# Performance work log

Measured on AMD Instinct MI355X. Metric: run time of the kernel, lower is better.

## Reference

```python
import jax, jax.numpy as jnp
import numpy as np

B, IN_C, OUT_C, H, W = 16, 64, 64, 128, 128
MIN_R, MAX_R, BASE, SCALE = 1, 6, 3, 3


def setup_inputs() -> dict:
    key = jax.random.key(0)
    k1, k2 = jax.random.split(key)
    x = jax.random.normal(k1, (B, IN_C, H, W), dtype=jnp.float32)
    # kaiming-uniform-ish scale for a 3x3 conv weight
    weight = jax.random.normal(k2, (OUT_C, IN_C, 3, 3), dtype=jnp.float32) * (1.0 / np.sqrt(IN_C * 9))
    # truncated-normal-style integer dilation per output channel (deterministic)
    rng = np.random.default_rng(0)
    offsets = np.clip(np.round(rng.normal(BASE, SCALE, size=OUT_C)), MIN_R, MAX_R).astype(np.int32)
    return {"x": x, "weight": weight, "offsets": offsets}


def _gsd_conv(x, weight, offs_np):
    # Per-channel dilation conv: group channels by dilation, conv each group
    # (dilation=o, padding=o keeps HxW), scatter back to original channel order.
    out = jnp.zeros((x.shape[0], weight.shape[0], x.shape[2], x.shape[3]), dtype=x.dtype)
    for o in np.unique(offs_np):
        idx = np.nonzero(offs_np == o)[0]          # static channel indices for this dilation
        w = weight[idx]                             # [g, in_c, 3, 3]
        o = int(o)
        y = jax.lax.conv_general_dilated(
            x, w,
            window_strides=(1, 1),
            padding=[(o, o), (o, o)],
            rhs_dilation=(o, o),
            dimension_numbers=("NCHW", "OIHW", "NCHW"),
        )                                           # [B, g, H, W]
        out = out.at[:, idx].set(y)
    return out


def reference(x, weight, offsets):
    offs_np = np.asarray(offsets)
    return _gsd_conv(x, weight, offs_np)
```

## Files before the change

kernel.cpp:

```cpp
#include <hip/hip_runtime.h>


#define HW_ 128
#define C_ 64
#define B_ 16
#define EX 44
#define EY 28
#define MAX_ITEMS 12
#define WS_WPACK_OFF 1024


typedef __attribute__((ext_vector_type(8))) short short8;
typedef __attribute__((ext_vector_type(16))) float floatx16;

__device__ __forceinline__ unsigned bf16rne(float f) {
  unsigned u = __float_as_uint(f);
  return (u + 0x7FFFu + ((u >> 16) & 1u)) >> 16;
}

__global__ __launch_bounds__(256) void gsd_setup(
    const int* __restrict__ offsets, const float* __restrict__ w,
    int* __restrict__ desc, uint4* __restrict__ wpack) {
  __shared__ int sd[128];
  __shared__ int soffs[C_];
  const int tid = threadIdx.x;
  if (tid < C_) soffs[tid] = offsets[tid];
  __syncthreads();
  if (tid == 0) {
    int p = 0;
    for (int d = 1; d <= 6; ++d)
      for (int c = 0; c < C_; ++c)
        if (soffs[c] == d) sd[p++] = c;
    int ni = 0;
    for (int t = 0; t < 2; ++t) {
      int cnt = 0, prev = -1;
      for (int m = 0; m < 32; ++m) {
        const int dd = soffs[sd[t * 32 + m]];
        if (dd != prev && cnt < 6 && ni < MAX_ITEMS) {
          sd[66 + t * 6 + cnt] = dd;
          sd[78 + t * 6 + cnt] = ni;
          sd[91 + ni * 2] = t;
          sd[92 + ni * 2] = dd;
          ++ni;
          ++cnt;
          prev = dd;
        }
      }
      sd[64 + t] = cnt;
    }
    sd[90] = ni;
  }
  __syncthreads();

  const int bid = blockIdx.x;
  if (bid == 0) {
    if (tid < 91) desc[tid] = sd[tid];
    return;
  }
  const int wix = bid - 1;
  if (wix >= sd[90]) return;
  const int o = sd[91 + wix * 2];
  const int dit = sd[92 + wix * 2];

  for (int i = tid; i < 4 * 9 * 64; i += 256) {
    const int ks = i / 576;
    const int r = i % 576;
    const int tap = r >> 6;
    const int lane = r & 63;
    const int m = lane & 31, h = lane >> 5;
    const int oc = sd[o * 32 + m];
    const bool act = (soffs[oc] == dit);
    unsigned ww[4];
    for (int jj = 0; jj < 4; ++jj) {
      float v0 = 0.f, v1 = 0.f;
      if (act) {
        const int ic0 = ks * 16 + h * 8 + jj * 2;
        v0 = w[(oc * C_ + ic0) * 9 + tap];
        v1 = w[(oc * C_ + ic0 + 1) * 9 + tap];
      }
      ww[jj] = bf16rne(v0) | (bf16rne(v1) << 16);
    }
    wpack[(size_t)wix * 2304 + i] = make_uint4(ww[0], ww[1], ww[2], ww[3]);
  }
}

__global__ __launch_bounds__(512, 4) void gsd_conv(
    const float* __restrict__ x, const int* __restrict__ desc,
    const uint4* __restrict__ wpack, float* __restrict__ out) {
  const int tid = threadIdx.x;
  const int gxid = blockIdx.x;
  const int b = gxid >> 5;
  const int yt = (gxid >> 2) & 7;
  const int xt = gxid & 3;
  const int y0 = yt * 16, x0 = xt * 32;

  const int lane = tid & 63;
  const int n = lane & 31;
  const int h = lane >> 5;
  const int wv = tid >> 6;
  const int o = wv >> 2;
  const int rq = wv & 3;

  const int slx = tid & 63;
  const int sq = (tid >> 6) & 3;
  const int sy2 = tid >> 8;

  __shared__ unsigned ldsbuf[EY * EX * 8];

  floatx16 acc[4];
#pragma unroll
  for (int rt = 0; rt < 4; ++rt)
#pragma unroll
    for (int e = 0; e < 16; ++e) acc[rt][e] = 0.f;

  const float* xb = x + (size_t)b * (C_ * HW_ * HW_);
  const int gx = x0 - 6 + slx;
  const int gxc = gx < 0 ? 0 : (gx > 127 ? 127 : gx);
  const bool xin = ((unsigned)gx < 128u) & (slx < EX);

  const int cnt = __builtin_amdgcn_readfirstlane(desc[64 + o]);

  for (int ks = 0; ks < 4; ++ks) {
    if (ks) __syncthreads();
    const float* xp = xb + (size_t)(ks * 16 + sq * 4) * (HW_ * HW_);
#pragma unroll 2
    for (int yy = sy2; yy < EY; yy += 2) {
      const int gy = y0 - 6 + yy;
      const int gyc = gy < 0 ? 0 : (gy > 127 ? 127 : gy);
      const bool ok = xin & ((unsigned)gy < 128u);
      const float* p = xp + gyc * HW_ + gxc;
      float v0 = p[0];
      float v1 = p[HW_ * HW_];
      float v2 = p[2 * HW_ * HW_];
      float v3 = p[3 * HW_ * HW_];
      if (!ok) { v0 = v1 = v2 = v3 = 0.f; }
      const unsigned lo = bf16rne(v0) | (bf16rne(v1) << 16);
      const unsigned hi = bf16rne(v2) | (bf16rne(v3) << 16);
      if (slx < EX) {
        const int pix = yy * EX + slx;
        const int dws =
            pix * 8 + (((sq >> 1) ^ (pix & 1)) << 2) + ((sq & 1) << 1);
        *reinterpret_cast<uint2*>(&ldsbuf[dws]) = make_uint2(lo, hi);
      }
    }
    __syncthreads();

    for (int s = 0; s < cnt; ++s) {
      const int d = __builtin_amdgcn_readfirstlane(desc[66 + o * 6 + s]);
      const int wix = __builtin_amdgcn_readfirstlane(desc[78 + o * 6 + s]);
      const uint4* wp = wpack + ((size_t)wix * 4 + ks) * 576 + lane;
#pragma unroll
      for (int tap = 0; tap < 9; ++tap) {
        const int ky = tap / 3 - 1, kx = tap % 3 - 1;
        const short8 af = __builtin_bit_cast(short8, wp[tap * 64]);
        const int pybase = rq * 4 + ky * d + 6;
        const int pxb = n + kx * d + 6;
#pragma unroll
        for (int rt = 0; rt < 4; ++rt) {
          const int pix = (pybase + rt) * EX + pxb;
          const int dws = (pix << 3) + ((h ^ (pix & 1)) << 2);
          const short8 bf = *reinterpret_cast<const short8*>(&ldsbuf[dws]);
          acc[rt] = __builtin_amdgcn_mfma_f32_32x32x16_bf16(af, bf, acc[rt],
                                                            0, 0, 0);
        }
      }
    }
  }

  int oc[16];
#pragma unroll
  for (int reg = 0; reg < 16; ++reg) {
    const int row = (reg & 3) + 8 * (reg >> 2) + 4 * h;
    oc[reg] = desc[o * 32 + row];
  }
#pragma unroll
  for (int rt = 0; rt < 4; ++rt) {
    const int y = y0 + rq * 4 + rt;
#pragma unroll
    for (int reg = 0; reg < 16; ++reg) {
      out[((size_t)(b * C_ + oc[reg]) * HW_ + y) * HW_ + x0 + n] =
          acc[rt][reg];
    }
  }
}

extern "C" void kernel_launch(void* const* d_in, const int* in_sizes, int n_in,
                              void* d_out, int out_size, void* d_ws, size_t ws_size,
                              hipStream_t stream) {
  const float* x = (const float*)d_in[0];
  const float* w = (const float*)d_in[1];
  const int* offsets = (const int*)d_in[2];
  float* out = (float*)d_out;

  int* desc = (int*)d_ws;
  uint4* wpack = (uint4*)((char*)d_ws + WS_WPACK_OFF);

  gsd_setup<<<dim3(1 + MAX_ITEMS), 256, 0, stream>>>(offsets, w, desc, wpack);
  gsd_conv<<<dim3(B_ * 8 * 4), 512, 0, stream>>>(x, desc, wpack, out);
}
```

Measured before the change: 216.4 us.

## Pre-convert input to padded channel-last bf16 and stage via global_load_lds

Adds a prep pass that converts x once into a zero-padded NHWC bf16 buffer in workspace. The conv kernel then copies tiles straight into LDS with global_load_lds instead of doing strided fp32 loads, per-element clamping and bf16 conversion in every block. The LDS swizzle changes to match the new copy pattern, and the channel sort becomes a parallel rank computation. The cost is an extra full pass over x and a larger workspace; the old path is kept as a fallback when the workspace is too small.

```diff
diff --git a/kernel.cpp b/kernel.cpp
--- a/kernel.cpp
+++ b/kernel.cpp
@@ -6,8 +6,12 @@
 #define B_ 16
 #define EX 44
 #define EY 28
+#define NPIX (EY * EX)
+#define PADW 140
 #define MAX_ITEMS 12
 #define WS_WPACK_OFF 1024
+#define WS_XB16_OFF (1 << 20)
+#define XB16_BYTES ((size_t)B_ * PADW * PADW * C_ * 2)
 
 
 typedef __attribute__((ext_vector_type(8))) short short8;
@@ -18,19 +22,64 @@
   return (u + 0x7FFFu + ((u >> 16) & 1u)) >> 16;
 }
 
-__global__ __launch_bounds__(256) void gsd_setup(
-    const int* __restrict__ offsets, const float* __restrict__ w,
-    int* __restrict__ desc, uint4* __restrict__ wpack) {
+#define GLOAD_LDS16(g, l)                                   \
+  __builtin_amdgcn_global_load_lds(                         \
+      (const __attribute__((address_space(1))) void*)(g),   \
+      (__attribute__((address_space(3))) void*)(l), 16, 0, 0)
+
+__global__ __launch_bounds__(256) void gsd_prep(
+    const float* __restrict__ x, const int* __restrict__ offsets,
+    const float* __restrict__ w, int* __restrict__ desc,
+    uint4* __restrict__ wpack, unsigned short* __restrict__ xb16,
+    const int nrow) {
+  const int bid = blockIdx.x;
+  const int tid = threadIdx.x;
+
+  if (bid < nrow) {
+    const int b = bid / PADW, py = bid - b * PADW;
+    uint4* o4 = (uint4*)(xb16 + (size_t)bid * (PADW * C_));
+    const uint4 z = make_uint4(0, 0, 0, 0);
+    if (py < 6 || py >= PADW - 6) {
+      for (int i = tid; i < PADW * C_ / 8; i += 256) o4[i] = z;
+      return;
+    }
+    if (tid < 48) o4[tid] = z;
+    else if (tid < 96) o4[1024 + tid] = z;
+    const int y = py - 6;
+    __shared__ unsigned l32[128 * 33];
+    const int xx = tid & 127, ph = tid >> 7;
+    const float* xp = x + (size_t)b * (C_ * HW_ * HW_) + y * HW_ + xx;
+#pragma unroll 4
+    for (int p = ph; p < 32; p += 2) {
+      const float v0 = xp[(2 * p) * (HW_ * HW_)];
+      const float v1 = xp[(2 * p + 1) * (HW_ * HW_)];
+      l32[xx * 33 + p] = bf16rne(v0) | (bf16rne(v1) << 16);
+    }
+    __syncthreads();
+#pragma unroll 4
+    for (int ch = tid; ch < 1024; ch += 256) {
+      const int px = ch >> 3, qq = ch & 7;
+      const unsigned* s = &l32[px * 33 + qq * 4];
+      o4[48 + ch] = make_uint4(s[0], s[1], s[2], s[3]);
+    }
+    return;
+  }
+
   __shared__ int sd[128];
   __shared__ int soffs[C_];
-  const int tid = threadIdx.x;
   if (tid < C_) soffs[tid] = offsets[tid];
   __syncthreads();
+  if (tid < C_) {
+    const int key = soffs[tid];
+    int rank = 0;
+    for (int c = 0; c < C_; ++c) {
+      const int kc = soffs[c];
+      rank += (int)((kc < key) | ((kc == key) & (c < tid)));
+    }
+    sd[rank] = tid;
+  }
+  __syncthreads();
   if (tid == 0) {
-    int p = 0;
-    for (int d = 1; d <= 6; ++d)
-      for (int c = 0; c < C_; ++c)
-        if (soffs[c] == d) sd[p++] = c;
     int ni = 0;
     for (int t = 0; t < 2; ++t) {
       int cnt = 0, prev = -1;
@@ -52,12 +101,12 @@
   }
   __syncthreads();
 
-  const int bid = blockIdx.x;
-  if (bid == 0) {
+  const int sbid = bid - nrow;
+  if (sbid == 0) {
     if (tid < 91) desc[tid] = sd[tid];
     return;
   }
-  const int wix = bid - 1;
+  const int wix = sbid - 1;
   if (wix >= sd[90]) return;
   const int o = sd[91 + wix * 2];
   const int dit = sd[92 + wix * 2];
@@ -67,14 +116,14 @@
     const int r = i % 576;
     const int tap = r >> 6;
     const int lane = r & 63;
-    const int m = lane & 31, h = lane >> 5;
+    const int m = lane & 31, hh = lane >> 5;
     const int oc = sd[o * 32 + m];
     const bool act = (soffs[oc] == dit);
     unsigned ww[4];
     for (int jj = 0; jj < 4; ++jj) {
       float v0 = 0.f, v1 = 0.f;
       if (act) {
-        const int ic0 = ks * 16 + h * 8 + jj * 2;
+        const int ic0 = ks * 16 + hh * 8 + jj * 2;
         v0 = w[(oc * C_ + ic0) * 9 + tap];
         v1 = w[(oc * C_ + ic0 + 1) * 9 + tap];
       }
@@ -84,9 +133,11 @@
   }
 }
 
+template <bool PRE>
 __global__ __launch_bounds__(512, 4) void gsd_conv(
-    const float* __restrict__ x, const int* __restrict__ desc,
-    const uint4* __restrict__ wpack, float* __restrict__ out) {
+    const float* __restrict__ x, const unsigned short* __restrict__ xb16,
+    const int* __restrict__ desc, const uint4* __restrict__ wpack,
+    float* __restrict__ out) {
   const int tid = threadIdx.x;
   const int gxid = blockIdx.x;
   const int b = gxid >> 5;
@@ -101,11 +152,7 @@
   const int o = wv >> 2;
   const int rq = wv & 3;
 
-  const int slx = tid & 63;
-  const int sq = (tid >> 6) & 3;
-  const int sy2 = tid >> 8;
-
-  __shared__ unsigned ldsbuf[EY * EX * 8];
+  __shared__ __align__(16) unsigned ldsbuf[40 * 256];
 
   floatx16 acc[4];
 #pragma unroll
@@ -113,34 +160,64 @@
 #pragma unroll
     for (int e = 0; e < 16; ++e) acc[rt][e] = 0.f;
 
-  const float* xb = x + (size_t)b * (C_ * HW_ * HW_);
-  const int gx = x0 - 6 + slx;
-  const int gxc = gx < 0 ? 0 : (gx > 127 ? 127 : gx);
-  const bool xin = ((unsigned)gx < 128u) & (slx < EX);
+  const unsigned short* xrow;
+  int srcoff[5];
+  if constexpr (PRE) {
+    xrow = xb16 + (size_t)b * (PADW * PADW * C_);
+#pragma unroll
+    for (int j = 0; j < 5; ++j) {
+      const int q = (wv + j * 8) * 64 + lane;
+      int pix = q >> 1;
+      if (pix > NPIX - 1) pix = NPIX - 1;
+      const int p = q & 1;
+      const int yy = pix / EX, xx = pix - yy * EX;
+      const int half = p ^ ((pix >> 2) & 1);
+      srcoff[j] = ((y0 + yy) * PADW + (x0 + xx)) * C_ + half * 8;
+    }
+  }
+  int slx, sq, sy2, gxc;
+  bool xin;
+  const float* xb;
+  if constexpr (!PRE) {
+    slx = tid & 63;
+    sq = (tid >> 6) & 3;
+    sy2 = tid >> 8;
+    xb = x + (size_t)b * (C_ * HW_ * HW_);
+    const int gx = x0 - 6 + slx;
+    gxc = gx < 0 ? 0 : (gx > 127 ? 127 : gx);
+    xin = ((unsigned)gx < 128u) & (slx < EX);
+  }
 
   const int cnt = __builtin_amdgcn_readfirstlane(desc[64 + o]);
 
   for (int ks = 0; ks < 4; ++ks) {
     if (ks) __syncthreads();
-    const float* xp = xb + (size_t)(ks * 16 + sq * 4) * (HW_ * HW_);
+    if constexpr (PRE) {
+#pragma unroll
+      for (int j = 0; j < 5; ++j) {
+        GLOAD_LDS16(xrow + srcoff[j] + ks * 16, &ldsbuf[(wv + j * 8) * 256]);
+      }
+    } else {
+      const float* xp = xb + (size_t)(ks * 16 + sq * 4) * (HW_ * HW_);
 #pragma unroll 2
-    for (int yy = sy2; yy < EY; yy += 2) {
-      const int gy = y0 - 6 + yy;
-      const int gyc = gy < 0 ? 0 : (gy > 127 ? 127 : gy);
-      const bool ok = xin & ((unsigned)gy < 128u);
-      const float* p = xp + gyc * HW_ + gxc;
-      float v0 = p[0];
-      float v1 = p[HW_ * HW_];
-      float v2 = p[2 * HW_ * HW_];
-      float v3 = p[3 * HW_ * HW_];
-      if (!ok) { v0 = v1 = v2 = v3 = 0.f; }
-      const unsigned lo = bf16rne(v0) | (bf16rne(v1) << 16);
-      const unsigned hi = bf16rne(v2) | (bf16rne(v3) << 16);
-      if (slx < EX) {
-        const int pix = yy * EX + slx;
-        const int dws =
-            pix * 8 + (((sq >> 1) ^ (pix & 1)) << 2) + ((sq & 1) << 1);
-        *reinterpret_cast<uint2*>(&ldsbuf[dws]) = make_uint2(lo, hi);
+      for (int yy = sy2; yy < EY; yy += 2) {
+        const int gy = y0 - 6 + yy;
+        const int gyc = gy < 0 ? 0 : (gy > 127 ? 127 : gy);
+        const bool ok = xin & ((unsigned)gy < 128u);
+        const float* p = xp + gyc * HW_ + gxc;
+        float v0 = p[0];
+        float v1 = p[HW_ * HW_];
+        float v2 = p[2 * HW_ * HW_];
+        float v3 = p[3 * HW_ * HW_];
+        if (!ok) { v0 = v1 = v2 = v3 = 0.f; }
+        const unsigned lo = bf16rne(v0) | (bf16rne(v1) << 16);
+        const unsigned hi = bf16rne(v2) | (bf16rne(v3) << 16);
+        if (slx < EX) {
+          const int pix = yy * EX + slx;
+          const int dws =
+              pix * 8 + (((sq >> 1) ^ ((pix >> 2) & 1)) << 2) + ((sq & 1) << 1);
+          *reinterpret_cast<uint2*>(&ldsbuf[dws]) = make_uint2(lo, hi);
+        }
       }
     }
     __syncthreads();
@@ -158,7 +235,7 @@
 #pragma unroll
         for (int rt = 0; rt < 4; ++rt) {
           const int pix = (pybase + rt) * EX + pxb;
-          const int dws = (pix << 3) + ((h ^ (pix & 1)) << 2);
+          const int dws = (pix << 3) + ((h ^ ((pix >> 2) & 1)) << 2);
           const short8 bf = *reinterpret_cast<const short8*>(&ldsbuf[dws]);
           acc[rt] = __builtin_amdgcn_mfma_f32_32x32x16_bf16(af, bf, acc[rt],
                                                             0, 0, 0);
@@ -185,8 +262,8 @@
 }
 
 extern "C" void kernel_launch(void* const* d_in, const int* in_sizes, int n_in,
-                              void* d_out, int out_size, void* d_ws, size_t ws_size,
-                              hipStream_t stream) {
+                              void* d_out, int out_size, void* d_ws,
+                              size_t ws_size, hipStream_t stream) {
   const float* x = (const float*)d_in[0];
   const float* w = (const float*)d_in[1];
   const int* offsets = (const int*)d_in[2];
@@ -194,7 +271,18 @@
 
   int* desc = (int*)d_ws;
   uint4* wpack = (uint4*)((char*)d_ws + WS_WPACK_OFF);
-
-  gsd_setup<<<dim3(1 + MAX_ITEMS), 256, 0, stream>>>(offsets, w, desc, wpack);
-  gsd_conv<<<dim3(B_ * 8 * 4), 512, 0, stream>>>(x, desc, wpack, out);
-}
+  unsigned short* xb16 = (unsigned short*)((char*)d_ws + WS_XB16_OFF);
+
+  const bool pre = ws_size >= (size_t)WS_XB16_OFF + XB16_BYTES;
+  const int nrow = pre ? B_ * PADW : 0;
+
+  gsd_prep<<<dim3(nrow + 1 + MAX_ITEMS), 256, 0, stream>>>(
+      x, offsets, w, desc, wpack, xb16, nrow);
+  if (pre) {
+    gsd_conv<true><<<dim3(B_ * 8 * 4), 512, 0, stream>>>(
+        x, xb16, desc, wpack, out);
+  } else {
+    gsd_conv<false><<<dim3(B_ * 8 * 4), 512, 0, stream>>>(
+        x, xb16, desc, wpack, out);
+  }
+}
```

Measured after the change: 217.2 us. No clear change (+0.3%).
